# Kernel tuning notes

Measured on AMD Instinct MI355X. Metric: run time of the kernel, lower is better.

## Reference

```python
import jax, jax.numpy as jnp
import numpy as np

N_NODES = 100000
N_EDGES = 1600000
F_IN = 64
HID = 64
N_CLASSES = 45
N_GRAPHS = 256


def gcn_conv(x, src, dst, W, b, n):
    # GCNConv with added self-loops and symmetric normalization (PyG semantics)
    h = x @ W  # [N, H]
    deg = jax.ops.segment_sum(jnp.ones(src.shape[0], h.dtype), dst, num_segments=n) + 1.0
    dinv = jax.lax.rsqrt(deg)  # deg^{-1/2}, deg >= 1 due to self loops
    coef = dinv[src] * dinv[dst]  # [E]
    msg = h[src] * coef[:, None]  # gather + scale
    agg = jax.ops.segment_sum(msg, dst, num_segments=n)  # scatter-add to dst
    agg = agg + h * (dinv * dinv)[:, None]  # self-loop contribution
    return agg + b


def setup_inputs() -> dict:
    key = jax.random.key(0)
    ks = jax.random.split(key, 12)
    x = jax.random.normal(ks[0], (N_NODES, F_IN), dtype=jnp.float32)
    edge_index = jax.random.randint(ks[1], (2, N_EDGES), 0, N_NODES, dtype=jnp.int32)
    batch = jnp.sort(jax.random.randint(ks[2], (N_NODES,), 0, N_GRAPHS, dtype=jnp.int32))
    s1 = 1.0 / np.sqrt(F_IN)
    s2 = 1.0 / np.sqrt(HID)
    W1 = jax.random.uniform(ks[3], (F_IN, HID), jnp.float32, -s1, s1)
    b1 = jnp.zeros((HID,), jnp.float32)
    W2 = jax.random.uniform(ks[4], (HID, HID), jnp.float32, -s2, s2)
    b2 = jnp.zeros((HID,), jnp.float32)
    W3 = jax.random.uniform(ks[5], (HID, HID), jnp.float32, -s2, s2)
    b3 = jnp.zeros((HID,), jnp.float32)
    Wl = jax.random.uniform(ks[6], (HID, N_CLASSES), jnp.float32, -s2, s2)
    bl = jnp.zeros((N_CLASSES,), jnp.float32)
    return {"x": x, "edge_index": edge_index, "batch": batch,
            "W1": W1, "b1": b1, "W2": W2, "b2": b2, "W3": W3, "b3": b3,
            "Wl": Wl, "bl": bl}


def reference(x, edge_index, batch, W1, b1, W2, b2, W3, b3, Wl, bl):
    n = x.shape[0]
    src, dst = edge_index[0], edge_index[1]
    h = jax.nn.relu(gcn_conv(x, src, dst, W1, b1, n))
    h = jax.nn.relu(gcn_conv(h, src, dst, W2, b2, n))
    h = gcn_conv(h, src, dst, W3, b3, n)
    # global mean pool over graph segments
    sums = jax.ops.segment_sum(h, batch, num_segments=N_GRAPHS)  # [G, H]
    cnts = jax.ops.segment_sum(jnp.ones(n, h.dtype), batch, num_segments=N_GRAPHS)
    pooled = sums / jnp.maximum(cnts, 1.0)[:, None]
    # dropout is identity in eval mode
    return pooled @ Wl + bl  # [G, num_classes]
```

## Files before the change

### kernel.cpp

```cpp
#include <hip/hip_runtime.h>
#include <hip/hip_bf16.h>

#define N_NODES   100000
#define N_EDGES   1600000
#define F_IN      64
#define HID       64
#define N_CLASSES 45
#define N_GRAPHS  256
#define SB        392
#define NPB       256
#define CAP       4608
#define WPB       72
#define CHUNK     4096
#define NCHUNK    391
#define NZB       192
#define GEMM_GRID 3125
#define AGGE_GRID 7056
#define NZB2      192
#define ZLEN4_F   1600000
#define ZLEN4_A   1604096

__device__ __forceinline__ float rl_f(float v, int k) {
    return __uint_as_float(__builtin_amdgcn_readlane(__float_as_uint(v), k));
}
__device__ __forceinline__ int rl_i(int v, int k) {
    return __builtin_amdgcn_readlane(v, k);
}
__device__ __forceinline__ unsigned short f2bf(float x) {
    unsigned u = __float_as_uint(x);
    unsigned r = u + 0x7FFFu + ((u >> 16) & 1u);
    return (unsigned short)(r >> 16);
}
__device__ __forceinline__ float bf2f(unsigned short h) {
    return __uint_as_float(((unsigned)h) << 16);
}

__global__ __launch_bounds__(256) void k_front(const int* __restrict__ src, const int* __restrict__ dst,
                                               int* __restrict__ bcur, int* __restrict__ binned,
                                               const float* __restrict__ x, const float* __restrict__ W1,
                                               unsigned short* __restrict__ P, float* __restrict__ zbase) {
    int bid = blockIdx.x;
    int t   = threadIdx.x;
    if (bid < NCHUNK) {
        __shared__ int stg[CHUNK];
        __shared__ unsigned short bkt[CHUNK];
        __shared__ int h[512], cur[512], off[512];
        __shared__ int ps[256];
        h[t] = 0; h[t + 256] = 0;
        __syncthreads();
        int base4 = bid * (CHUNK / 4);
        #pragma unroll
        for (int i = 0; i < CHUNK / 1024; i++) {
            int e4 = base4 + i * 256 + t;
            if (e4 < N_EDGES / 4) {
                int4 d = ((const int4*)dst)[e4];
                atomicAdd(&h[d.x >> 8], 1);
                atomicAdd(&h[d.y >> 8], 1);
                atomicAdd(&h[d.z >> 8], 1);
                atomicAdd(&h[d.w >> 8], 1);
            }
        }
        __syncthreads();
        int a0 = h[2 * t], a1 = h[2 * t + 1];
        ps[t] = a0 + a1;
        __syncthreads();
        for (int o = 1; o < 256; o <<= 1) {
            int v = (t >= o) ? ps[t - o] : 0;
            __syncthreads();
            if (t >= o) ps[t] += v;
            __syncthreads();
        }
        int pex = ps[t] - (a0 + a1);
        int e0 = pex, e1 = pex + a0;
        cur[2 * t] = e0; cur[2 * t + 1] = e1;
        if (2 * t < SB && a0 > 0)
            off[2 * t] = (2 * t) * CAP + atomicAdd(&bcur[2 * t], a0) - e0;
        if (2 * t + 1 < SB && a1 > 0)
            off[2 * t + 1] = (2 * t + 1) * CAP + atomicAdd(&bcur[2 * t + 1], a1) - e1;
        __syncthreads();
        int total = ps[255];
        #pragma unroll
        for (int i = 0; i < CHUNK / 1024; i++) {
            int e4 = base4 + i * 256 + t;
            if (e4 < N_EDGES / 4) {
                int4 d  = ((const int4*)dst)[e4];
                int4 s4 = ((const int4*)src)[e4];
                int q;
                q = atomicAdd(&cur[d.x >> 8], 1); stg[q] = s4.x | ((d.x & 255) << 17); bkt[q] = (unsigned short)(d.x >> 8);
                q = atomicAdd(&cur[d.y >> 8], 1); stg[q] = s4.y | ((d.y & 255) << 17); bkt[q] = (unsigned short)(d.y >> 8);
                q = atomicAdd(&cur[d.z >> 8], 1); stg[q] = s4.z | ((d.z & 255) << 17); bkt[q] = (unsigned short)(d.z >> 8);
                q = atomicAdd(&cur[d.w >> 8], 1); stg[q] = s4.w | ((d.w & 255) << 17); bkt[q] = (unsigned short)(d.w >> 8);
            }
        }
        __syncthreads();
        for (int i = t; i < total; i += 256) {
            int b = bkt[i];
            binned[off[b] + i] = stg[i];
        }
    } else if (bid < NCHUNK + NZB) {
        float4 z = make_float4(0.f, 0.f, 0.f, 0.f);
        float4* zp = (float4*)zbase;
        int zb = bid - NCHUNK;
        for (long i = (long)zb * 256 + t; i < (long)ZLEN4_F; i += (long)NZB * 256)
            zp[i] = z;
    } else {
        int gbid = bid - NCHUNK - NZB;
        int lane = t & 63;
        int wv   = t >> 6;
        int base = gbid * 32 + wv * 8;
        float xr[8], acc[8];
        #pragma unroll
        for (int r = 0; r < 8; r++) {
            xr[r]  = x[(size_t)(base + r) * 64 + lane];
            acc[r] = 0.f;
        }
        for (int kb = 0; kb < 64; kb += 8) {
            float wb[8];
            #pragma unroll
            for (int j = 0; j < 8; j++) wb[j] = W1[(kb + j) * 64 + lane];
            #pragma unroll
            for (int j = 0; j < 8; j++) {
                #pragma unroll
                for (int r = 0; r < 8; r++)
                    acc[r] = fmaf(rl_f(xr[r], kb + j), wb[j], acc[r]);
            }
        }
        #pragma unroll
        for (int r = 0; r < 8; r++)
            P[(size_t)(base + r) * 64 + lane] = f2bf(acc[r]);
    }
}

__global__ __launch_bounds__(256) void k_bcsr(const int* __restrict__ binned, const int* __restrict__ bcur,
                                              float* __restrict__ dinv, float* __restrict__ dinv2,
                                              int* __restrict__ csr) {
    __shared__ int h[NPB];
    __shared__ int ts[NPB];
    int t = threadIdx.x;
    int b = blockIdx.x;
    int nb0  = b << 8;
    int ebeg = b * CAP;
    int ecnt = bcur[b]; if (ecnt > CAP) ecnt = CAP;
    h[t] = 0;
    __syncthreads();
    for (int i = t; i < ecnt; i += 256)
        atomicAdd(&h[binned[ebeg + i] >> 17], 1);
    __syncthreads();
    int c = h[t];
    ts[t] = c;
    __syncthreads();
    for (int o = 1; o < 256; o <<= 1) {
        int v = (t >= o) ? ts[t - o] : 0;
        __syncthreads();
        if (t >= o) ts[t] += v;
        __syncthreads();
    }
    int excl = ts[t] - c + ebeg;
    int n = nb0 + t;
    if (n < N_NODES) {
        float inv = 1.0f / (float)(c + 1);
        dinv2[n] = inv;
        dinv[n]  = sqrtf(inv);
    }
    __syncthreads();
    h[t] = excl;
    __syncthreads();
    for (int i = t; i < ecnt; i += 256) {
        int p = binned[ebeg + i];
        int q = atomicAdd(&h[p >> 17], 1);
        csr[q] = p;
    }
}

template<bool POOLI>
__global__ __launch_bounds__(256) void k_gemm(const float* __restrict__ E,
                                              unsigned short* P,
                                              const float* __restrict__ W,
                                              const float* __restrict__ bprev,
                                              const float* __restrict__ bcurr,
                                              const float* __restrict__ dinv2,
                                              const int* __restrict__ batch,
                                              float* __restrict__ pool) {
    int lane = threadIdx.x & 63;
    int wv   = threadIdx.x >> 6;
    int base = blockIdx.x * 32 + wv * 8;
    float bp = bprev[lane];
    float xr[8], acc[8];
    #pragma unroll
    for (int r = 0; r < 8; r++) {
        int n = base + r;
        float hp = bf2f(P[(size_t)n * 64 + lane]);
        float a  = E[(size_t)n * 64 + lane] + fmaf(hp, dinv2[n], bp);
        xr[r]  = fmaxf(a, 0.f);
        acc[r] = 0.f;
    }
    for (int kb = 0; kb < 64; kb += 8) {
        float wb[8];
        #pragma unroll
        for (int j = 0; j < 8; j++) wb[j] = W[(kb + j) * 64 + lane];
        #pragma unroll
        for (int j = 0; j < 8; j++) {
            #pragma unroll
            for (int r = 0; r < 8; r++)
                acc[r] = fmaf(rl_f(xr[r], kb + j), wb[j], acc[r]);
        }
    }
    #pragma unroll
    for (int r = 0; r < 8; r++)
        P[(size_t)(base + r) * 64 + lane] = f2bf(acc[r]);
    if (POOLI) {
        float bv = bcurr[lane];
        float d2[8];
        #pragma unroll
        for (int r = 0; r < 8; r++) d2[r] = dinv2[base + r];
        int g0 = batch[base], g7 = batch[base + 7];
        if (g0 == g7) {
            float s = 0.f;
            #pragma unroll
            for (int r = 0; r < 8; r++) s += fmaf(acc[r], d2[r], bv);
            atomicAdd(&pool[g0 * 64 + lane], s);
        } else {
            #pragma unroll
            for (int r = 0; r < 8; r++) {
                int g = batch[base + r];
                atomicAdd(&pool[g * 64 + lane], fmaf(acc[r], d2[r], bv));
            }
        }
    }
}

template<bool POOLEP, bool ZROLE>
__global__ __launch_bounds__(256, 8) void k_agge(const unsigned short* __restrict__ Hbuf,
                                                 const int* __restrict__ csr,
                                                 const int* __restrict__ bcur,
                                                 const float* __restrict__ dinv,
                                                 const int* __restrict__ batch,
                                                 float* __restrict__ Out,
                                                 float* __restrict__ zbase) {
    int t = threadIdx.x;
    if (ZROLE && blockIdx.x >= AGGE_GRID) {
        float4 z = make_float4(0.f, 0.f, 0.f, 0.f);
        float4* zp = (float4*)zbase;
        int zb = blockIdx.x - AGGE_GRID;
        for (long i = (long)zb * 256 + t; i < (long)ZLEN4_A; i += (long)NZB2 * 256)
            zp[i] = z;
        return;
    }
    int wv   = t >> 6;
    int lane = t & 63;
    int wid  = blockIdx.x * 4 + wv;
    int b    = wid / WPB;
    int lw   = wid - b * WPB;
    int used = bcur[b]; if (used > CAP) used = CAP;
    int e0   = lw * 64;
    int rem  = used - e0;
    if (rem <= 0) return;
    if (rem > 64) rem = 64;
    int base = b * CAP + e0;

    int p = 0;
    float cv = 0.f;
    if (lane < rem) {
        p  = csr[base + lane];
        cv = dinv[p & 0x1FFFF];
    }
    int sv = p & 0x1FFFF;
    int dv = p >> 17;

    auto flush = [&](int dl, float a) {
        int dst = (b << 8) + dl;
        if (dst < N_NODES) {
            float val = dinv[dst] * a;
            if (POOLEP) {
                int g = batch[dst];
                atomicAdd(&Out[g * 64 + lane], val);
            } else {
                atomicAdd(&Out[(size_t)dst * 64 + lane], val);
            }
        }
    };

    int dprev = rl_i(dv, 0);
    float acc = 0.f;
    int j = 0;
    for (; j + 16 <= rem; j += 16) {
        unsigned short u[16];
        #pragma unroll
        for (int i = 0; i < 16; i++) {
            int s = rl_i(sv, j + i);
            u[i] = Hbuf[(size_t)s * 64 + lane];
        }
        #pragma unroll
        for (int i = 0; i < 16; i++) {
            int   d = rl_i(dv, j + i);
            float c = rl_f(cv, j + i);
            if (d != dprev) { flush(dprev, acc); acc = 0.f; dprev = d; }
            acc = fmaf(bf2f(u[i]), c, acc);
        }
    }
    for (; j < rem; j++) {
        int   s0 = rl_i(sv, j);
        float c0 = rl_f(cv, j);
        int   d0 = rl_i(dv, j);
        unsigned short u0 = Hbuf[(size_t)s0 * 64 + lane];
        if (d0 != dprev) { flush(dprev, acc); acc = 0.f; dprev = d0; }
        acc = fmaf(bf2f(u0), c0, acc);
    }
    flush(dprev, acc);
}

__device__ __forceinline__ int lbound(const int* __restrict__ a, int n, int v) {
    int lo = 0, hi = n;
    while (lo < hi) { int m = (lo + hi) >> 1; if (a[m] < v) lo = m + 1; else hi = m; }
    return lo;
}

__global__ __launch_bounds__(64) void k_cls(const float* __restrict__ pool, const int* __restrict__ batch,
                                            const float* __restrict__ Wl, const float* __restrict__ bl,
                                            float* __restrict__ out) {
    __shared__ float pm[64];
    __shared__ int bounds[2];
    int g = blockIdx.x;
    int t = threadIdx.x;
    if (t < 2) bounds[t] = lbound(batch, N_NODES, g + t);
    __syncthreads();
    float cnt = (float)(bounds[1] - bounds[0]);
    pm[t] = pool[g * 64 + t] / fmaxf(cnt, 1.0f);
    __syncthreads();
    if (t < N_CLASSES) {
        float o = bl[t];
        #pragma unroll
        for (int k = 0; k < HID; k++) o = fmaf(pm[k], Wl[k * N_CLASSES + t], o);
        out[g * N_CLASSES + t] = o;
    }
}


extern "C" void kernel_launch(void* const* d_in, const int* in_sizes, int n_in,
                              void* d_out, int out_size, void* d_ws, size_t ws_size,
                              hipStream_t stream) {
    const float* x     = (const float*)d_in[0];
    const int*   eidx  = (const int*)  d_in[1];
    const int*   batch = (const int*)  d_in[2];
    const float* W1 = (const float*)d_in[3];
    const float* b1 = (const float*)d_in[4];
    const float* W2 = (const float*)d_in[5];
    const float* b2 = (const float*)d_in[6];
    const float* W3 = (const float*)d_in[7];
    const float* b3 = (const float*)d_in[8];
    const float* Wl = (const float*)d_in[9];
    const float* bl = (const float*)d_in[10];
    const int* src = eidx;
    const int* dst = eidx + N_EDGES;

    char* p = (char*)d_ws;
    auto alloc = [&](size_t bytes) -> void* {
        void* r = (void*)p;
        p += (bytes + 255) & ~(size_t)255;
        return r;
    };
    float* dinv  = (float*)alloc((size_t)N_NODES * 4);
    float* dinv2 = (float*)alloc((size_t)N_NODES * 4);
    int*   csr   = (int*)  alloc((size_t)SB * CAP * 4);
    unsigned short* P = (unsigned short*)alloc((size_t)N_NODES * 64 * 2);
    float* E1    = (float*)alloc((size_t)N_NODES * 64 * 4);
    float* pool  = (float*)alloc((size_t)N_GRAPHS * 64 * 4);
    float* E2    = (float*)alloc((size_t)N_NODES * 64 * 4);
    int*   bcur  = (int*)  alloc((size_t)SB * 4);
    int*   binned = (int*) alloc((size_t)SB * CAP * 4);

    const int front_grid = NCHUNK + NZB + GEMM_GRID;

    hipMemsetAsync(bcur, 0, (size_t)SB * 4, stream);
    k_front<<<front_grid, 256, 0, stream>>>(src, dst, bcur, binned, x, W1, P, E1);
    k_bcsr <<<SB, 256, 0, stream>>>(binned, bcur, dinv, dinv2, csr);

    k_agge<false, true ><<<AGGE_GRID + NZB2, 256, 0, stream>>>(P, csr, bcur, dinv, batch, E1, pool);
    k_gemm<false><<<GEMM_GRID, 256, 0, stream>>>(E1, P, W2, b1, nullptr, dinv2, batch, nullptr);
    k_agge<false, false><<<AGGE_GRID, 256, 0, stream>>>(P, csr, bcur, dinv, batch, E2, nullptr);
    k_gemm<true ><<<GEMM_GRID, 256, 0, stream>>>(E2, P, W3, b2, b3, dinv2, batch, pool);
    k_agge<true , false><<<AGGE_GRID, 256, 0, stream>>>(P, csr, bcur, dinv, batch, pool, nullptr);

    k_cls<<<N_GRAPHS, 64, 0, stream>>>(pool, batch, Wl, bl, (float*)d_out);
}
```

Before: 368.7 us.

## Split edges into destination-aligned windows so aggregation stores instead of atomically adding

The CSR build kernel now packs each bucket's destination-sorted edges into 64-edge windows that never split a destination node. The per-node aggregation kernels then write each destination's sum with a plain store rather than an atomicAdd. Only nodes with zero in-degree are zero-filled, which removes the bulk zeroing of E1/E2 that k_front and k_agge used to do. The risks: degrees above 64 are clamped, a bucket with more than 84 windows drops its extra edges, and one serial thread builds the windows in every block.

```diff
diff --git a/kernel.cpp b/kernel.cpp
--- a/kernel.cpp
+++ b/kernel.cpp
@@ -10,15 +10,11 @@
 #define SB        392
 #define NPB       256
 #define CAP       4608
-#define WPB       72
 #define CHUNK     4096
 #define NCHUNK    391
-#define NZB       192
 #define GEMM_GRID 3125
-#define AGGE_GRID 7056
-#define NZB2      192
-#define ZLEN4_F   1600000
-#define ZLEN4_A   1604096
+#define WSLOT     84
+#define WGRID     8232
 
 __device__ __forceinline__ float rl_f(float v, int k) {
     return __uint_as_float(__builtin_amdgcn_readlane(__float_as_uint(v), k));
@@ -38,7 +34,7 @@
 __global__ __launch_bounds__(256) void k_front(const int* __restrict__ src, const int* __restrict__ dst,
                                                int* __restrict__ bcur, int* __restrict__ binned,
                                                const float* __restrict__ x, const float* __restrict__ W1,
-                                               unsigned short* __restrict__ P, float* __restrict__ zbase) {
+                                               unsigned short* __restrict__ P) {
     int bid = blockIdx.x;
     int t   = threadIdx.x;
     if (bid < NCHUNK) {
@@ -97,14 +93,8 @@
             int b = bkt[i];
             binned[off[b] + i] = stg[i];
         }
-    } else if (bid < NCHUNK + NZB) {
-        float4 z = make_float4(0.f, 0.f, 0.f, 0.f);
-        float4* zp = (float4*)zbase;
-        int zb = bid - NCHUNK;
-        for (long i = (long)zb * 256 + t; i < (long)ZLEN4_F; i += (long)NZB * 256)
-            zp[i] = z;
     } else {
-        int gbid = bid - NCHUNK - NZB;
+        int gbid = bid - NCHUNK;
         int lane = t & 63;
         int wv   = t >> 6;
         int base = gbid * 32 + wv * 8;
@@ -133,9 +123,12 @@
 
 __global__ __launch_bounds__(256) void k_bcsr(const int* __restrict__ binned, const int* __restrict__ bcur,
                                               float* __restrict__ dinv, float* __restrict__ dinv2,
-                                              int* __restrict__ csr) {
+                                              int* __restrict__ csr, unsigned* __restrict__ windows,
+                                              float* __restrict__ E1, float* __restrict__ E2) {
     __shared__ int h[NPB];
     __shared__ int ts[NPB];
+    __shared__ unsigned wstage[WSLOT];
+    __shared__ int s_nw;
     int t = threadIdx.x;
     int b = blockIdx.x;
     int nb0  = b << 8;
@@ -161,7 +154,32 @@
         float inv = 1.0f / (float)(c + 1);
         dinv2[n] = inv;
         dinv[n]  = sqrtf(inv);
-    }
+        if (c == 0) {
+            float4 z = make_float4(0.f, 0.f, 0.f, 0.f);
+            #pragma unroll
+            for (int i = 0; i < 16; i++) {
+                ((float4*)E1)[(size_t)n * 16 + i] = z;
+                ((float4*)E2)[(size_t)n * 16 + i] = z;
+            }
+        }
+    }
+    __syncthreads();
+    if (t == 0) {
+        int nw = 0, cs = ebeg, cc = 0;
+        for (int i = 0; i < NPB; i++) {
+            int ci = h[i]; if (ci > 64) ci = 64;
+            if (ci == 0) continue;
+            if (cc + ci > 64) {
+                if (cc > 0 && nw < WSLOT) wstage[nw++] = (unsigned)cs | ((unsigned)cc << 21);
+                cs += cc; cc = 0;
+            }
+            cc += ci;
+        }
+        if (cc > 0 && nw < WSLOT) wstage[nw++] = (unsigned)cs | ((unsigned)cc << 21);
+        s_nw = nw;
+    }
+    __syncthreads();
+    if (t < WSLOT) windows[b * WSLOT + t] = (t < s_nw) ? wstage[t] : 0u;
     __syncthreads();
     h[t] = excl;
     __syncthreads();
@@ -229,54 +247,40 @@
     }
 }
 
-template<bool POOLEP, bool ZROLE>
+template<bool POOLEP>
 __global__ __launch_bounds__(256, 8) void k_agge(const unsigned short* __restrict__ Hbuf,
                                                  const int* __restrict__ csr,
-                                                 const int* __restrict__ bcur,
+                                                 const unsigned* __restrict__ windows,
                                                  const float* __restrict__ dinv,
                                                  const int* __restrict__ batch,
-                                                 float* __restrict__ Out,
-                                                 float* __restrict__ zbase) {
-    int t = threadIdx.x;
-    if (ZROLE && blockIdx.x >= AGGE_GRID) {
-        float4 z = make_float4(0.f, 0.f, 0.f, 0.f);
-        float4* zp = (float4*)zbase;
-        int zb = blockIdx.x - AGGE_GRID;
-        for (long i = (long)zb * 256 + t; i < (long)ZLEN4_A; i += (long)NZB2 * 256)
-            zp[i] = z;
-        return;
-    }
+                                                 float* __restrict__ Out) {
+    int t    = threadIdx.x;
     int wv   = t >> 6;
     int lane = t & 63;
     int wid  = blockIdx.x * 4 + wv;
-    int b    = wid / WPB;
-    int lw   = wid - b * WPB;
-    int used = bcur[b]; if (used > CAP) used = CAP;
-    int e0   = lw * 64;
-    int rem  = used - e0;
-    if (rem <= 0) return;
-    if (rem > 64) rem = 64;
-    int base = b * CAP + e0;
+    unsigned w = windows[wid];
+    if (w == 0) return;
+    int start = (int)(w & 0x1FFFFFu);
+    int rem   = (int)(w >> 21);
+    int b     = start / CAP;
 
     int p = 0;
     float cv = 0.f;
     if (lane < rem) {
-        p  = csr[base + lane];
+        p  = csr[start + lane];
         cv = dinv[p & 0x1FFFF];
     }
     int sv = p & 0x1FFFF;
     int dv = p >> 17;
 
-    auto flush = [&](int dl, float a) {
+    auto flush1 = [&](int dl, float a) {
         int dst = (b << 8) + dl;
-        if (dst < N_NODES) {
-            float val = dinv[dst] * a;
-            if (POOLEP) {
-                int g = batch[dst];
-                atomicAdd(&Out[g * 64 + lane], val);
-            } else {
-                atomicAdd(&Out[(size_t)dst * 64 + lane], val);
-            }
+        float val = dinv[dst] * a;
+        if (POOLEP) {
+            int g = batch[dst];
+            atomicAdd(&Out[g * 64 + lane], val);
+        } else {
+            Out[(size_t)dst * 64 + lane] = val;
         }
     };
 
@@ -294,7 +298,7 @@
         for (int i = 0; i < 16; i++) {
             int   d = rl_i(dv, j + i);
             float c = rl_f(cv, j + i);
-            if (d != dprev) { flush(dprev, acc); acc = 0.f; dprev = d; }
+            if (d != dprev) { flush1(dprev, acc); acc = 0.f; dprev = d; }
             acc = fmaf(bf2f(u[i]), c, acc);
         }
     }
@@ -303,10 +307,10 @@
         float c0 = rl_f(cv, j);
         int   d0 = rl_i(dv, j);
         unsigned short u0 = Hbuf[(size_t)s0 * 64 + lane];
-        if (d0 != dprev) { flush(dprev, acc); acc = 0.f; dprev = d0; }
+        if (d0 != dprev) { flush1(dprev, acc); acc = 0.f; dprev = d0; }
         acc = fmaf(bf2f(u0), c0, acc);
     }
-    flush(dprev, acc);
+    flush1(dprev, acc);
 }
 
 __device__ __forceinline__ int lbound(const int* __restrict__ a, int n, int v) {
@@ -368,18 +372,18 @@
     float* E2    = (float*)alloc((size_t)N_NODES * 64 * 4);
     int*   bcur  = (int*)  alloc((size_t)SB * 4);
     int*   binned = (int*) alloc((size_t)SB * CAP * 4);
-
-    const int front_grid = NCHUNK + NZB + GEMM_GRID;
+    unsigned* windows = (unsigned*)alloc((size_t)SB * WSLOT * 4);
 
     hipMemsetAsync(bcur, 0, (size_t)SB * 4, stream);
-    k_front<<<front_grid, 256, 0, stream>>>(src, dst, bcur, binned, x, W1, P, E1);
-    k_bcsr <<<SB, 256, 0, stream>>>(binned, bcur, dinv, dinv2, csr);
-
-    k_agge<false, true ><<<AGGE_GRID + NZB2, 256, 0, stream>>>(P, csr, bcur, dinv, batch, E1, pool);
+    hipMemsetAsync(pool, 0, (size_t)N_GRAPHS * 64 * 4, stream);
+    k_front<<<NCHUNK + GEMM_GRID, 256, 0, stream>>>(src, dst, bcur, binned, x, W1, P);
+    k_bcsr <<<SB, 256, 0, stream>>>(binned, bcur, dinv, dinv2, csr, windows, E1, E2);
+
+    k_agge<false><<<WGRID, 256, 0, stream>>>(P, csr, windows, dinv, batch, E1);
     k_gemm<false><<<GEMM_GRID, 256, 0, stream>>>(E1, P, W2, b1, nullptr, dinv2, batch, nullptr);
-    k_agge<false, false><<<AGGE_GRID, 256, 0, stream>>>(P, csr, bcur, dinv, batch, E2, nullptr);
+    k_agge<false><<<WGRID, 256, 0, stream>>>(P, csr, windows, dinv, batch, E2);
     k_gemm<true ><<<GEMM_GRID, 256, 0, stream>>>(E2, P, W3, b2, b3, dinv2, batch, pool);
-    k_agge<true , false><<<AGGE_GRID, 256, 0, stream>>>(P, csr, bcur, dinv, batch, pool, nullptr);
+    k_agge<true ><<<WGRID, 256, 0, stream>>>(P, csr, windows, dinv, batch, pool);
 
     k_cls<<<N_GRAPHS, 64, 0, stream>>>(pool, batch, Wl, bl, (float*)d_out);
 }
```

After: 402.5 us. 9.2% more time.

## Precompute per-edge coefficients and issue all 64 gathers before accumulating

Applied to the files above, without the earlier changes.

Adds a k_coef pass that computes dinv[src]*dinv[dst] once per CSR slot, so the three aggregation kernels read one coefficient per edge. This drops the dinv gather per edge and the dinv[dst] multiply in each flush. Full 64-edge waves now issue all 64 bf16 row gathers up front, behind a sched barrier, to expose more memory-level parallelism. Occupancy is lowered to 5 waves per SIMD to fit the larger register array. The costs are an extra kernel launch and a coefficient buffer the size of the CSR.

```diff
diff --git a/kernel.cpp b/kernel.cpp
--- a/kernel.cpp
+++ b/kernel.cpp
@@ -19,6 +19,7 @@
 #define NZB2      192
 #define ZLEN4_F   1600000
 #define ZLEN4_A   1604096
+#define COEF_GRID 1764
 
 __device__ __forceinline__ float rl_f(float v, int k) {
     return __uint_as_float(__builtin_amdgcn_readlane(__float_as_uint(v), k));
@@ -170,6 +171,33 @@
         int q = atomicAdd(&h[p >> 17], 1);
         csr[q] = p;
     }
+}
+
+__global__ __launch_bounds__(256) void k_coef(const int* __restrict__ csr, const float* __restrict__ dinv,
+                                              float* __restrict__ coef) {
+    int i4 = blockIdx.x * 256 + threadIdx.x;
+    int b  = (i4 >> 10) * 4096 / CAP;
+    b = (i4 * 4) / CAP;
+    int nb0 = b << 8;
+    int4 p = ((const int4*)csr)[i4];
+    float4 c;
+    {
+        unsigned u0 = (unsigned)p.x; int s = (int)(u0 & 0x1FFFFu); int d = nb0 + (int)((u0 >> 17) & 0xFFu);
+        c.x = dinv[s < N_NODES ? s : 0] * dinv[d < N_NODES ? d : 0];
+    }
+    {
+        unsigned u0 = (unsigned)p.y; int s = (int)(u0 & 0x1FFFFu); int d = nb0 + (int)((u0 >> 17) & 0xFFu);
+        c.y = dinv[s < N_NODES ? s : 0] * dinv[d < N_NODES ? d : 0];
+    }
+    {
+        unsigned u0 = (unsigned)p.z; int s = (int)(u0 & 0x1FFFFu); int d = nb0 + (int)((u0 >> 17) & 0xFFu);
+        c.z = dinv[s < N_NODES ? s : 0] * dinv[d < N_NODES ? d : 0];
+    }
+    {
+        unsigned u0 = (unsigned)p.w; int s = (int)(u0 & 0x1FFFFu); int d = nb0 + (int)((u0 >> 17) & 0xFFu);
+        c.w = dinv[s < N_NODES ? s : 0] * dinv[d < N_NODES ? d : 0];
+    }
+    ((float4*)coef)[i4] = c;
 }
 
 template<bool POOLI>
@@ -230,10 +258,10 @@
 }
 
 template<bool POOLEP, bool ZROLE>
-__global__ __launch_bounds__(256, 8) void k_agge(const unsigned short* __restrict__ Hbuf,
+__global__ __launch_bounds__(256, 5) void k_agge(const unsigned short* __restrict__ Hbuf,
                                                  const int* __restrict__ csr,
                                                  const int* __restrict__ bcur,
-                                                 const float* __restrict__ dinv,
+                                                 const float* __restrict__ coef,
                                                  const int* __restrict__ batch,
                                                  float* __restrict__ Out,
                                                  float* __restrict__ zbase) {
@@ -262,51 +290,71 @@
     float cv = 0.f;
     if (lane < rem) {
         p  = csr[base + lane];
-        cv = dinv[p & 0x1FFFF];
-    }
-    int sv = p & 0x1FFFF;
+        cv = coef[base + lane];
+    }
     int dv = p >> 17;
 
-    auto flush = [&](int dl, float a) {
+    auto flush1 = [&](int dl, float a) {
         int dst = (b << 8) + dl;
         if (dst < N_NODES) {
-            float val = dinv[dst] * a;
             if (POOLEP) {
                 int g = batch[dst];
-                atomicAdd(&Out[g * 64 + lane], val);
+                atomicAdd(&Out[g * 64 + lane], a);
             } else {
-                atomicAdd(&Out[(size_t)dst * 64 + lane], val);
+                atomicAdd(&Out[(size_t)dst * 64 + lane], a);
             }
         }
     };
 
-    int dprev = rl_i(dv, 0);
-    float acc = 0.f;
-    int j = 0;
-    for (; j + 16 <= rem; j += 16) {
-        unsigned short u[16];
-        #pragma unroll
-        for (int i = 0; i < 16; i++) {
-            int s = rl_i(sv, j + i);
-            u[i] = Hbuf[(size_t)s * 64 + lane];
-        }
-        #pragma unroll
-        for (int i = 0; i < 16; i++) {
-            int   d = rl_i(dv, j + i);
-            float c = rl_f(cv, j + i);
-            if (d != dprev) { flush(dprev, acc); acc = 0.f; dprev = d; }
+    if (rem == 64) {
+        const unsigned short* Hl = Hbuf + lane;
+        unsigned short u[64];
+        #pragma unroll
+        for (int i = 0; i < 64; i++) {
+            unsigned s = (unsigned)(rl_i(p, i) & 0x1FFFF);
+            u[i] = Hl[(size_t)s << 6];
+        }
+        __builtin_amdgcn_sched_barrier(0);
+        int dprev = rl_i(dv, 0);
+        float acc = 0.f;
+        #pragma unroll
+        for (int i = 0; i < 64; i++) {
+            int   d = rl_i(dv, i);
+            float c = rl_f(cv, i);
+            if (d != dprev) { flush1(dprev, acc); acc = 0.f; dprev = d; }
             acc = fmaf(bf2f(u[i]), c, acc);
         }
-    }
-    for (; j < rem; j++) {
-        int   s0 = rl_i(sv, j);
-        float c0 = rl_f(cv, j);
-        int   d0 = rl_i(dv, j);
-        unsigned short u0 = Hbuf[(size_t)s0 * 64 + lane];
-        if (d0 != dprev) { flush(dprev, acc); acc = 0.f; dprev = d0; }
-        acc = fmaf(bf2f(u0), c0, acc);
-    }
-    flush(dprev, acc);
+        flush1(dprev, acc);
+    } else {
+        int sv = p & 0x1FFFF;
+        int dprev = rl_i(dv, 0);
+        float acc = 0.f;
+        int j = 0;
+        for (; j + 16 <= rem; j += 16) {
+            unsigned short u[16];
+            #pragma unroll
+            for (int i = 0; i < 16; i++) {
+                int s = rl_i(sv, j + i);
+                u[i] = Hbuf[(size_t)s * 64 + lane];
+            }
+            #pragma unroll
+            for (int i = 0; i < 16; i++) {
+                int   d = rl_i(dv, j + i);
+                float c = rl_f(cv, j + i);
+                if (d != dprev) { flush1(dprev, acc); acc = 0.f; dprev = d; }
+                acc = fmaf(bf2f(u[i]), c, acc);
+            }
+        }
+        for (; j < rem; j++) {
+            int   s0 = rl_i(sv, j);
+            float c0 = rl_f(cv, j);
+            int   d0 = rl_i(dv, j);
+            unsigned short u0 = Hbuf[(size_t)s0 * 64 + lane];
+            if (d0 != dprev) { flush1(dprev, acc); acc = 0.f; dprev = d0; }
+            acc = fmaf(bf2f(u0), c0, acc);
+        }
+        flush1(dprev, acc);
+    }
 }
 
 __device__ __forceinline__ int lbound(const int* __restrict__ a, int n, int v) {
@@ -368,18 +416,20 @@
     float* E2    = (float*)alloc((size_t)N_NODES * 64 * 4);
     int*   bcur  = (int*)  alloc((size_t)SB * 4);
     int*   binned = (int*) alloc((size_t)SB * CAP * 4);
+    float* coef  = (float*)alloc((size_t)SB * CAP * 4);
 
     const int front_grid = NCHUNK + NZB + GEMM_GRID;
 
     hipMemsetAsync(bcur, 0, (size_t)SB * 4, stream);
     k_front<<<front_grid, 256, 0, stream>>>(src, dst, bcur, binned, x, W1, P, E1);
     k_bcsr <<<SB, 256, 0, stream>>>(binned, bcur, dinv, dinv2, csr);
-
-    k_agge<false, true ><<<AGGE_GRID + NZB2, 256, 0, stream>>>(P, csr, bcur, dinv, batch, E1, pool);
+    k_coef <<<COEF_GRID, 256, 0, stream>>>(csr, dinv, coef);
+
+    k_agge<false, true ><<<AGGE_GRID + NZB2, 256, 0, stream>>>(P, csr, bcur, coef, batch, E1, pool);
     k_gemm<false><<<GEMM_GRID, 256, 0, stream>>>(E1, P, W2, b1, nullptr, dinv2, batch, nullptr);
-    k_agge<false, false><<<AGGE_GRID, 256, 0, stream>>>(P, csr, bcur, dinv, batch, E2, nullptr);
+    k_agge<false, false><<<AGGE_GRID, 256, 0, stream>>>(P, csr, bcur, coef, batch, E2, nullptr);
     k_gemm<true ><<<GEMM_GRID, 256, 0, stream>>>(E2, P, W3, b2, b3, dinv2, batch, pool);
-    k_agge<true , false><<<AGGE_GRID, 256, 0, stream>>>(P, csr, bcur, dinv, batch, pool, nullptr);
+    k_agge<true , false><<<AGGE_GRID, 256, 0, stream>>>(P, csr, bcur, coef, batch, pool, nullptr);
 
     k_cls<<<N_GRAPHS, 64, 0, stream>>>(pool, batch, Wl, bl, (float*)d_out);
 }
```

Result: slower. 386.5 us (+4.8%).

## Prescale features by dinv[src] so edge aggregation skips per-edge coefficient gather

Applied to the files above, without the earlier changes.

Folds the source-side normalization dinv[src] into the stored bf16 feature table. This is done in k_bcsr for layer 1 and in the GEMM epilogue for later layers, so the aggregation kernel sums raw rows instead of gathering dinv per edge and doing an FMA. Segment boundaries are now found once per wave with a ballot mask instead of comparing readlane destinations for every edge. In exchange, k_bcsr does an extra read-modify-write pass over P, and the prescaled values go through one more bf16 rounding. The self-loop term now uses hp*dinv, which equals the old dinv2 factor because hp is already scaled by dinv.

```diff
diff --git a/kernel.cpp b/kernel.cpp
--- a/kernel.cpp
+++ b/kernel.cpp
@@ -34,6 +34,11 @@
 __device__ __forceinline__ float bf2f(unsigned short h) {
     return __uint_as_float(((unsigned)h) << 16);
 }
+__device__ __forceinline__ unsigned scale2(unsigned u, float dv) {
+    float lo = __uint_as_float(u << 16) * dv;
+    float hi = __uint_as_float(u & 0xFFFF0000u) * dv;
+    return (((unsigned)f2bf(hi)) << 16) | (unsigned)f2bf(lo);
+}
 
 __global__ __launch_bounds__(256) void k_front(const int* __restrict__ src, const int* __restrict__ dst,
                                                int* __restrict__ bcur, int* __restrict__ binned,
@@ -133,9 +138,10 @@
 
 __global__ __launch_bounds__(256) void k_bcsr(const int* __restrict__ binned, const int* __restrict__ bcur,
                                               float* __restrict__ dinv, float* __restrict__ dinv2,
-                                              int* __restrict__ csr) {
+                                              int* __restrict__ csr, unsigned short* __restrict__ P) {
     __shared__ int h[NPB];
     __shared__ int ts[NPB];
+    __shared__ float sdv[NPB];
     int t = threadIdx.x;
     int b = blockIdx.x;
     int nb0  = b << 8;
@@ -157,11 +163,14 @@
     }
     int excl = ts[t] - c + ebeg;
     int n = nb0 + t;
+    float dval = 0.f;
     if (n < N_NODES) {
         float inv = 1.0f / (float)(c + 1);
         dinv2[n] = inv;
-        dinv[n]  = sqrtf(inv);
-    }
+        dval     = sqrtf(inv);
+        dinv[n]  = dval;
+    }
+    sdv[t] = dval;
     __syncthreads();
     h[t] = excl;
     __syncthreads();
@@ -169,6 +178,17 @@
         int p = binned[ebeg + i];
         int q = atomicAdd(&h[p >> 17], 1);
         csr[q] = p;
+    }
+    for (int i = t; i < NPB * 8; i += 256) {
+        int row = i >> 3;
+        int nn  = nb0 + row;
+        if (nn >= N_NODES) break;
+        float dv = sdv[row];
+        uint4* pp = (uint4*)P + (size_t)nn * 8 + (i & 7);
+        uint4 v = *pp;
+        v.x = scale2(v.x, dv); v.y = scale2(v.y, dv);
+        v.z = scale2(v.z, dv); v.w = scale2(v.w, dv);
+        *pp = v;
     }
 }
 
@@ -178,6 +198,7 @@
                                               const float* __restrict__ W,
                                               const float* __restrict__ bprev,
                                               const float* __restrict__ bcurr,
+                                              const float* __restrict__ dinv,
                                               const float* __restrict__ dinv2,
                                               const int* __restrict__ batch,
                                               float* __restrict__ pool) {
@@ -185,12 +206,14 @@
     int wv   = threadIdx.x >> 6;
     int base = blockIdx.x * 32 + wv * 8;
     float bp = bprev[lane];
-    float xr[8], acc[8];
+    float xr[8], acc[8], dn[8];
+    #pragma unroll
+    for (int r = 0; r < 8; r++) dn[r] = dinv[base + r];
     #pragma unroll
     for (int r = 0; r < 8; r++) {
         int n = base + r;
         float hp = bf2f(P[(size_t)n * 64 + lane]);
-        float a  = E[(size_t)n * 64 + lane] + fmaf(hp, dinv2[n], bp);
+        float a  = E[(size_t)n * 64 + lane] + fmaf(hp, dn[r], bp);
         xr[r]  = fmaxf(a, 0.f);
         acc[r] = 0.f;
     }
@@ -207,7 +230,7 @@
     }
     #pragma unroll
     for (int r = 0; r < 8; r++)
-        P[(size_t)(base + r) * 64 + lane] = f2bf(acc[r]);
+        P[(size_t)(base + r) * 64 + lane] = f2bf(acc[r] * dn[r]);
     if (POOLI) {
         float bv = bcurr[lane];
         float d2[8];
@@ -259,15 +282,17 @@
     int base = b * CAP + e0;
 
     int p = 0;
-    float cv = 0.f;
-    if (lane < rem) {
-        p  = csr[base + lane];
-        cv = dinv[p & 0x1FFFF];
-    }
+    if (lane < rem) p = csr[base + lane];
     int sv = p & 0x1FFFF;
     int dv = p >> 17;
 
-    auto flush = [&](int dl, float a) {
+    int dvp = __shfl_up(dv, 1);
+    unsigned long long m0 = __ballot(dv != dvp);
+    unsigned mlo = __builtin_amdgcn_readfirstlane((unsigned)m0);
+    unsigned mhi = __builtin_amdgcn_readfirstlane((unsigned)(m0 >> 32));
+    unsigned long long mask = ((((unsigned long long)mhi) << 32) | mlo) & ~1ull;
+
+    auto flush1 = [&](int dl, float a) {
         int dst = (b << 8) + dl;
         if (dst < N_NODES) {
             float val = dinv[dst] * a;
@@ -280,7 +305,7 @@
         }
     };
 
-    int dprev = rl_i(dv, 0);
+    int cur = rl_i(dv, 0);
     float acc = 0.f;
     int j = 0;
     for (; j + 16 <= rem; j += 16) {
@@ -292,21 +317,19 @@
         }
         #pragma unroll
         for (int i = 0; i < 16; i++) {
-            int   d = rl_i(dv, j + i);
-            float c = rl_f(cv, j + i);
-            if (d != dprev) { flush(dprev, acc); acc = 0.f; dprev = d; }
-            acc = fmaf(bf2f(u[i]), c, acc);
+            if ((mask >> (j + i)) & 1) {
+                flush1(cur, acc); acc = 0.f; cur = rl_i(dv, j + i);
+            }
+            acc += bf2f(u[i]);
         }
     }
     for (; j < rem; j++) {
-        int   s0 = rl_i(sv, j);
-        float c0 = rl_f(cv, j);
-        int   d0 = rl_i(dv, j);
+        int s0 = rl_i(sv, j);
         unsigned short u0 = Hbuf[(size_t)s0 * 64 + lane];
-        if (d0 != dprev) { flush(dprev, acc); acc = 0.f; dprev = d0; }
-        acc = fmaf(bf2f(u0), c0, acc);
-    }
-    flush(dprev, acc);
+        if ((mask >> j) & 1) { flush1(cur, acc); acc = 0.f; cur = rl_i(dv, j); }
+        acc += bf2f(u0);
+    }
+    flush1(cur, acc);
 }
 
 __device__ __forceinline__ int lbound(const int* __restrict__ a, int n, int v) {
@@ -373,12 +396,12 @@
 
     hipMemsetAsync(bcur, 0, (size_t)SB * 4, stream);
     k_front<<<front_grid, 256, 0, stream>>>(src, dst, bcur, binned, x, W1, P, E1);
-    k_bcsr <<<SB, 256, 0, stream>>>(binned, bcur, dinv, dinv2, csr);
+    k_bcsr <<<SB, 256, 0, stream>>>(binned, bcur, dinv, dinv2, csr, P);
 
     k_agge<false, true ><<<AGGE_GRID + NZB2, 256, 0, stream>>>(P, csr, bcur, dinv, batch, E1, pool);
-    k_gemm<false><<<GEMM_GRID, 256, 0, stream>>>(E1, P, W2, b1, nullptr, dinv2, batch, nullptr);
+    k_gemm<false><<<GEMM_GRID, 256, 0, stream>>>(E1, P, W2, b1, nullptr, dinv, dinv2, batch, nullptr);
     k_agge<false, false><<<AGGE_GRID, 256, 0, stream>>>(P, csr, bcur, dinv, batch, E2, nullptr);
-    k_gemm<true ><<<GEMM_GRID, 256, 0, stream>>>(E2, P, W3, b2, b3, dinv2, batch, pool);
+    k_gemm<true ><<<GEMM_GRID, 256, 0, stream>>>(E2, P, W3, b2, b3, dinv, dinv2, batch, pool);
     k_agge<true , false><<<AGGE_GRID, 256, 0, stream>>>(P, csr, bcur, dinv, batch, pool, nullptr);
 
     k_cls<<<N_GRAPHS, 64, 0, stream>>>(pool, batch, Wl, bl, (float*)d_out);
```

Result: no change. 363.5 us (-1.4%).
